# Performance work log

Hardware: AMD Instinct MI355X
Metric: run time of the kernel (lower is better)

The kernel has to match this reference:

```python
import jax, jax.numpy as jnp
import numpy as np

N_NODES = 50000
N_EDGES = 1600000
ATOM_F = 64
FP_SIZE = 2048
N_GRAPHS = 2000


def setup_inputs() -> dict:
    key = jax.random.key(0)
    ks = jax.random.split(key, 12)
    s = 1.0 / np.sqrt(ATOM_F)
    x = jax.random.normal(ks[0], (N_NODES, ATOM_F), dtype=jnp.float32)
    H1_w = jax.random.normal(ks[1], (ATOM_F, ATOM_F), dtype=jnp.float32) * s
    H1_b = jnp.zeros((ATOM_F,), dtype=jnp.float32)
    W1_w = jax.random.normal(ks[2], (FP_SIZE, ATOM_F), dtype=jnp.float32) * s
    W1_b = jnp.zeros((FP_SIZE,), dtype=jnp.float32)
    H2_w = jax.random.normal(ks[3], (ATOM_F, ATOM_F), dtype=jnp.float32) * s
    H2_b = jnp.zeros((ATOM_F,), dtype=jnp.float32)
    W2_w = jax.random.normal(ks[4], (FP_SIZE, ATOM_F), dtype=jnp.float32) * s
    W2_b = jnp.zeros((FP_SIZE,), dtype=jnp.float32)
    edge_index = jax.random.randint(ks[5], (2, N_EDGES), 0, N_NODES, dtype=jnp.int64)
    batch = jnp.sort(jax.random.randint(ks[6], (N_NODES,), 0, N_GRAPHS, dtype=jnp.int64))
    return {
        "x": x,
        "H1_w": H1_w, "H1_b": H1_b, "W1_w": W1_w, "W1_b": W1_b,
        "H2_w": H2_w, "H2_b": H2_b, "W2_w": W2_w, "W2_b": W2_b,
        "edge_index": edge_index,
        "batch": batch,
        "num_graphs": N_GRAPHS,
    }


def reference(x, H1_w, H1_b, W1_w, W1_b, H2_w, H2_b, W2_w, W2_b,
              edge_index, batch, num_graphs):
    n = x.shape[0]
    src, dst = edge_index[0], edge_index[1]

    def loop(h, Hw, Hb, Ww, Wb):
        # sum aggregation over incoming edges; '+ h' accounts for add_self_loops
        agg = jax.ops.segment_sum(h[src], dst, num_segments=n) + h
        upd = jax.nn.sigmoid(agg @ Hw.T + Hb)          # [N, atom_features]
        fp = jax.nn.softmax(upd @ Ww.T + Wb, axis=-1)  # [N, fp_size]
        return upd, fp

    h1, fp1 = loop(x, H1_w, H1_b, W1_w, W1_b)
    _, fp2 = loop(h1, H2_w, H2_b, W2_w, W2_b)
    fingerprint = fp1 + fp2
    # pool per-node fingerprints into per-graph fingerprints
    return jax.ops.segment_sum(fingerprint, batch, num_segments=num_graphs)
```

## Files before the change

### kernel.cpp

```cpp
#include <hip/hip_runtime.h>
#include <hip/hip_bf16.h>

#define AF 64
#define NFP 2048
#define MAXG 4

typedef __attribute__((ext_vector_type(8))) short bf16x8;
typedef __attribute__((ext_vector_type(4))) float f32x4;

__device__ __forceinline__ ushort f2bf(float f) {
    unsigned u = __float_as_uint(f);
    return (ushort)((u + 0x7FFF + ((u >> 16) & 1)) >> 16);
}
__device__ __forceinline__ float bf2f(ushort u) {
    return __uint_as_float((unsigned)u << 16);
}

__global__ __launch_bounds__(256) void hist_kernel(
    const int* __restrict__ keys, int* __restrict__ counts, int n)
{
    int e = blockIdx.x * 256 + threadIdx.x;
    if (e < n) atomicAdd(&counts[keys[e]], 1);
}

__global__ __launch_bounds__(256) void hist_part_kernel(
    const int* __restrict__ dst, int* __restrict__ counts,
    int n_edges, int npr, int nchunks)
{
    int r = blockIdx.x & 7;
    int c = blockIdx.x >> 3;
    int lo = r * npr, hi = lo + npr;
    int per = (n_edges + nchunks - 1) / nchunks;
    int e0 = c * per;
    int e1 = e0 + per; if (e1 > n_edges) e1 = n_edges;
    for (int e = e0 + (int)threadIdx.x; e < e1; e += 256) {
        int d = dst[e];
        if (d >= lo && d < hi) atomicAdd(&counts[d], 1);
    }
}

__global__ __launch_bounds__(1024) void scan_kernel(int* data, int n)
{
    __shared__ int wsum[16];
    __shared__ int chunk_total;
    int t = threadIdx.x, lane = t & 63, w = t >> 6;
    int running = 0;
    for (int base = 0; base < n; base += 1024) {
        int i = base + t;
        int v = (i < n) ? data[i] : 0;
        int x = v;
        #pragma unroll
        for (int off = 1; off < 64; off <<= 1) {
            int y = __shfl_up(x, off);
            if (lane >= off) x += y;
        }
        if (lane == 63) wsum[w] = x;
        __syncthreads();
        if (t == 0) {
            int s = 0;
            #pragma unroll
            for (int q = 0; q < 16; ++q) { int tmp = wsum[q]; wsum[q] = s; s += tmp; }
            chunk_total = s;
        }
        __syncthreads();
        if (i < n) data[i] = x - v + wsum[w] + running;
        running += chunk_total;
        __syncthreads();
    }
    if (t == 0) data[n] = running;
}

__global__ __launch_bounds__(256) void scatter_part_kernel(
    const int* __restrict__ src, const int* __restrict__ dst,
    int* __restrict__ cursor, int* __restrict__ esrc,
    int n_edges, int npr, int nchunks)
{
    int r = blockIdx.x & 7;
    int c = blockIdx.x >> 3;
    int lo = r * npr, hi = lo + npr;
    int per = (n_edges + nchunks - 1) / nchunks;
    int e0 = c * per;
    int e1 = e0 + per; if (e1 > n_edges) e1 = n_edges;
    for (int e = e0 + (int)threadIdx.x; e < e1; e += 256) {
        int d = dst[e];
        if (d >= lo && d < hi) {
            int pos = atomicAdd(&cursor[d], 1);
            esrc[pos] = src[e];
        }
    }
}

__global__ __launch_bounds__(256) void f2bf_kernel(
    const float* __restrict__ W, ushort* __restrict__ Wbf, int n)
{
    int i = blockIdx.x * 256 + threadIdx.x;
    if (i < n) Wbf[i] = f2bf(W[i]);
}

__global__ __launch_bounds__(256) void agg_mlp_kernel(
    const ushort* __restrict__ hbf, const int* __restrict__ offsets,
    const int* __restrict__ esrc, const float* __restrict__ Hw,
    const float* __restrict__ Hb, ushort* __restrict__ outbf, int n_nodes)
{
    __shared__ float Hw_s[AF * 65];
    __shared__ __align__(16) float part[4][8][AF];
    __shared__ float a_red[4][AF];
    __shared__ float hb_s[AF];

    int t = threadIdx.x;
    for (int idx = t; idx < AF * AF; idx += 256) {
        int j = idx >> 6, k = idx & 63;
        Hw_s[j * 65 + k] = Hw[idx];
    }
    if (t < AF) hb_s[t] = Hb[t];

    int w = t >> 6, lane = t & 63;
    int sub = lane >> 3, f8 = lane & 7;
    int i = blockIdx.x * 4 + w;

    float acc[8] = {0.f, 0.f, 0.f, 0.f, 0.f, 0.f, 0.f, 0.f};
    if (i < n_nodes) {
        int o0 = offsets[i], o1 = offsets[i + 1];
        const int* ep = esrc + o0;
        int deg = o1 - o0;
        for (int j = 0; j < deg; j += 8) {
            int jj = j + sub;
            if (jj < deg) {
                int s = ep[jj];
                bf16x8 v = *(const bf16x8*)(hbf + (size_t)s * AF + f8 * 8);
                #pragma unroll
                for (int q = 0; q < 8; ++q) acc[q] += bf2f((ushort)v[q]);
            }
        }
    }
    *(float4*)&part[w][sub][f8 * 8]     = make_float4(acc[0], acc[1], acc[2], acc[3]);
    *(float4*)&part[w][sub][f8 * 8 + 4] = make_float4(acc[4], acc[5], acc[6], acc[7]);
    __syncthreads();

    if (i < n_nodes) {
        float val = bf2f(hbf[(size_t)i * AF + lane]);
        #pragma unroll
        for (int s8 = 0; s8 < 8; ++s8) val += part[w][s8][lane];
        a_red[w][lane] = val;
    }
    __syncthreads();

    if (i < n_nodes) {
        float z = hb_s[lane];
        #pragma unroll
        for (int k = 0; k < AF; ++k)
            z = fmaf(a_red[w][k], Hw_s[lane * 65 + k], z);
        float sg = 1.f / (1.f + __expf(-z));
        outbf[(size_t)i * AF + lane] = f2bf(sg);
    }
}

__global__ __launch_bounds__(256) void fp_node_pool_kernel(
    const ushort* __restrict__ updbf, const ushort* __restrict__ Wbf,
    const float* __restrict__ Wb, const int* __restrict__ batch,
    float* __restrict__ partial, float* __restrict__ out, int n_nodes)
{
    __shared__ float red[4][32];
    __shared__ float sden_s[32];
    __shared__ int   bat_s[32];
    __shared__ __align__(16) float pacc[MAXG][NFP];

    int t = threadIdx.x, wave = t >> 6, lane = t & 63;
    int G = lane >> 4, sl = lane & 15;
    int cw = wave * 512;
    int b = blockIdx.x;
    int i0 = b * 32;

    bf16x8 a00, a01, a10, a11;
    {
        const ushort* p0 = updbf + (size_t)(i0 + sl) * AF + G * 8;
        a00 = *(const bf16x8*)p0;
        a01 = *(const bf16x8*)(p0 + 32);
        const ushort* p1 = updbf + (size_t)(i0 + 16 + sl) * AF + G * 8;
        a10 = *(const bf16x8*)p1;
        a11 = *(const bf16x8*)(p1 + 32);
    }

    float s0[4] = {0.f, 0.f, 0.f, 0.f};
    float s1[4] = {0.f, 0.f, 0.f, 0.f};
    {
        const ushort* wp0 = Wbf + (size_t)(cw + sl) * AF + G * 8;
        bf16x8 nb0 = *(const bf16x8*)wp0;
        bf16x8 nb1 = *(const bf16x8*)(wp0 + 32);
        #pragma unroll 4
        for (int ct = 0; ct < 32; ++ct) {
            bf16x8 b0 = nb0, b1 = nb1;
            if (ct < 31) {
                const ushort* wp = Wbf + (size_t)(cw + (ct + 1) * 16 + sl) * AF + G * 8;
                nb0 = *(const bf16x8*)wp;
                nb1 = *(const bf16x8*)(wp + 32);
            }
            float bias = Wb[cw + ct * 16 + sl];
            f32x4 d0 = {0.f, 0.f, 0.f, 0.f};
            d0 = __builtin_amdgcn_mfma_f32_16x16x32_bf16(a00, b0, d0, 0, 0, 0);
            d0 = __builtin_amdgcn_mfma_f32_16x16x32_bf16(a01, b1, d0, 0, 0, 0);
            f32x4 d1 = {0.f, 0.f, 0.f, 0.f};
            d1 = __builtin_amdgcn_mfma_f32_16x16x32_bf16(a10, b0, d1, 0, 0, 0);
            d1 = __builtin_amdgcn_mfma_f32_16x16x32_bf16(a11, b1, d1, 0, 0, 0);
            #pragma unroll
            for (int r = 0; r < 4; ++r) {
                s0[r] += __expf(d0[r] + bias);
                s1[r] += __expf(d1[r] + bias);
            }
        }
    }
    #pragma unroll
    for (int mask = 1; mask <= 8; mask <<= 1) {
        #pragma unroll
        for (int r = 0; r < 4; ++r) {
            s0[r] += __shfl_xor(s0[r], mask);
            s1[r] += __shfl_xor(s1[r], mask);
        }
    }
    if (sl == 0) {
        #pragma unroll
        for (int r = 0; r < 4; ++r) {
            red[wave][G * 4 + r]      = s0[r];
            red[wave][16 + G * 4 + r] = s1[r];
        }
    }
    if (t < 32) {
        int n = i0 + t;
        bat_s[t] = batch[n < n_nodes ? n : (n_nodes - 1)];
    }
    __syncthreads();
    if (t < 32) {
        float s = red[0][t] + red[1][t] + red[2][t] + red[3][t];
        sden_s[t] = 1.f / s;
    }
    __syncthreads();

    int g_first = bat_s[0];
    int ng = bat_s[31] - g_first + 1;
    int ngl = ng < MAXG ? ng : MAXG;

    for (int gi = 0; gi < ngl; ++gi) {
        *(float4*)&pacc[gi][cw + lane * 8]     = make_float4(0.f, 0.f, 0.f, 0.f);
        *(float4*)&pacc[gi][cw + lane * 8 + 4] = make_float4(0.f, 0.f, 0.f, 0.f);
    }

    float sc0[4], sc1[4];
    int gl0[4], gl1[4];
    #pragma unroll
    for (int r = 0; r < 4; ++r) {
        int l0 = G * 4 + r, l1 = l0 + 16;
        sc0[r] = (i0 + l0 < n_nodes) ? sden_s[l0] : 0.f;
        sc1[r] = (i0 + l1 < n_nodes) ? sden_s[l1] : 0.f;
        gl0[r] = bat_s[l0];
        gl1[r] = bat_s[l1];
    }

    {
        const ushort* wp0 = Wbf + (size_t)(cw + sl) * AF + G * 8;
        bf16x8 nb0 = *(const bf16x8*)wp0;
        bf16x8 nb1 = *(const bf16x8*)(wp0 + 32);
        #pragma unroll 4
        for (int ct = 0; ct < 32; ++ct) {
            bf16x8 b0 = nb0, b1 = nb1;
            if (ct < 31) {
                const ushort* wp = Wbf + (size_t)(cw + (ct + 1) * 16 + sl) * AF + G * 8;
                nb0 = *(const bf16x8*)wp;
                nb1 = *(const bf16x8*)(wp + 32);
            }
            int col = cw + ct * 16 + sl;
            float bias = Wb[col];
            f32x4 d0 = {0.f, 0.f, 0.f, 0.f};
            d0 = __builtin_amdgcn_mfma_f32_16x16x32_bf16(a00, b0, d0, 0, 0, 0);
            d0 = __builtin_amdgcn_mfma_f32_16x16x32_bf16(a01, b1, d0, 0, 0, 0);
            f32x4 d1 = {0.f, 0.f, 0.f, 0.f};
            d1 = __builtin_amdgcn_mfma_f32_16x16x32_bf16(a10, b0, d1, 0, 0, 0);
            d1 = __builtin_amdgcn_mfma_f32_16x16x32_bf16(a11, b1, d1, 0, 0, 0);
            float e0[4], e1[4];
            #pragma unroll
            for (int r = 0; r < 4; ++r) {
                e0[r] = __expf(d0[r] + bias) * sc0[r];
                e1[r] = __expf(d1[r] + bias) * sc1[r];
            }
            for (int gi = 0; gi < ng; ++gi) {
                int g = g_first + gi;
                float c = 0.f;
                #pragma unroll
                for (int r = 0; r < 4; ++r) {
                    c += (gl0[r] == g) ? e0[r] : 0.f;
                    c += (gl1[r] == g) ? e1[r] : 0.f;
                }
                c += __shfl_xor(c, 16);
                c += __shfl_xor(c, 32);
                if (gi < MAXG) {
                    if (G == 0) pacc[gi][col] += c;
                } else if (G == 0) {
                    unsafeAtomicAdd(&out[(size_t)g * NFP + col], c);
                }
            }
        }
    }

    for (int gi = 0; gi < ng; ++gi) {
        float* row = partial + (size_t)(b + g_first + gi) * NFP;
        if (gi < MAXG) {
            *(float4*)&row[cw + lane * 8]     = *(float4*)&pacc[gi][cw + lane * 8];
            *(float4*)&row[cw + lane * 8 + 4] = *(float4*)&pacc[gi][cw + lane * 8 + 4];
        } else {
            *(float4*)&row[cw + lane * 8]     = make_float4(0.f, 0.f, 0.f, 0.f);
            *(float4*)&row[cw + lane * 8 + 4] = make_float4(0.f, 0.f, 0.f, 0.f);
        }
    }
}

__global__ __launch_bounds__(256) void fp_reduce_kernel(
    const float* __restrict__ partial, const int* __restrict__ goff,
    float* __restrict__ out)
{
    int g = blockIdx.x, t = threadIdx.x;
    int gs = goff[g], ge = goff[g + 1];
    if (ge <= gs) return;
    int b0 = gs >> 5, b1 = (ge - 1) >> 5;
    float4 acc0 = make_float4(0.f, 0.f, 0.f, 0.f);
    float4 acc1 = make_float4(0.f, 0.f, 0.f, 0.f);
    for (int b = b0; b <= b1; ++b) {
        const float* row = partial + (size_t)(b + g) * NFP;
        float4 v0 = *(const float4*)&row[t * 8];
        float4 v1 = *(const float4*)&row[t * 8 + 4];
        acc0.x += v0.x; acc0.y += v0.y; acc0.z += v0.z; acc0.w += v0.w;
        acc1.x += v1.x; acc1.y += v1.y; acc1.z += v1.z; acc1.w += v1.w;
    }
    float* po = &out[(size_t)g * NFP];
    float4 o0 = *(float4*)&po[t * 8];
    float4 o1 = *(float4*)&po[t * 8 + 4];
    o0.x += acc0.x; o0.y += acc0.y; o0.z += acc0.z; o0.w += acc0.w;
    o1.x += acc1.x; o1.y += acc1.y; o1.z += acc1.z; o1.w += acc1.w;
    *(float4*)&po[t * 8]     = o0;
    *(float4*)&po[t * 8 + 4] = o1;
}

extern "C" void kernel_launch(void* const* d_in, const int* in_sizes, int n_in,
                              void* d_out, int out_size, void* d_ws, size_t ws_size,
                              hipStream_t stream)
{
    const float* x    = (const float*)d_in[0];
    const float* H1_w = (const float*)d_in[1];
    const float* H1_b = (const float*)d_in[2];
    const float* W1_w = (const float*)d_in[3];
    const float* W1_b = (const float*)d_in[4];
    const float* H2_w = (const float*)d_in[5];
    const float* H2_b = (const float*)d_in[6];
    const float* W2_w = (const float*)d_in[7];
    const float* W2_b = (const float*)d_in[8];
    const int*   ei   = (const int*)d_in[9];
    const int*   batch= (const int*)d_in[10];

    const int n_nodes  = in_sizes[0] / AF;
    const int n_edges  = in_sizes[9] / 2;
    const int n_graphs = out_size / NFP;
    const int npad     = ((n_nodes + 127) / 128) * 128;
    const int* src = ei;
    const int* dst = ei + n_edges;
    float* out = (float*)d_out;

    const int fp_blocks = (n_nodes + 31) / 32;
    const int npairs    = fp_blocks + n_graphs + 1;

    ushort* xbf     = (ushort*)d_ws;
    ushort* ubf1    = xbf  + (size_t)npad * AF;
    ushort* ubf2    = ubf1 + (size_t)npad * AF;
    ushort* Wbf1    = ubf2 + (size_t)npad * AF;
    ushort* Wbf2    = Wbf1 + (size_t)NFP * AF;
    float*  partial = (float*)(Wbf2 + (size_t)NFP * AF);
    int*    offsets = (int*)(partial + (size_t)npairs * NFP);
    int*    cursor  = offsets + (n_nodes + 1);
    int*    goff    = cursor + (n_nodes + 1);
    int*    esrc    = goff + (n_graphs + 1);

    const int nb = (n_nodes + 255) / 256;
    const int mlp_blocks = (n_nodes + 3) / 4;
    const int wn = NFP * AF;
    const int xn = n_nodes * AF;
    const int npr = (n_nodes + 7) / 8;
    const int nchunks = 256;

    f2bf_kernel<<<(xn + 255) / 256, 256, 0, stream>>>(x, xbf, xn);
    f2bf_kernel<<<(wn + 255) / 256, 256, 0, stream>>>(W1_w, Wbf1, wn);
    f2bf_kernel<<<(wn + 255) / 256, 256, 0, stream>>>(W2_w, Wbf2, wn);
    hipMemsetAsync(out, 0, (size_t)out_size * sizeof(float), stream);
    hipMemsetAsync(xbf + (size_t)n_nodes * AF, 0,
                   (size_t)(npad - n_nodes) * AF * sizeof(ushort), stream);
    hipMemsetAsync(ubf1 + (size_t)n_nodes * AF, 0,
                   (size_t)(npad - n_nodes) * AF * sizeof(ushort), stream);
    hipMemsetAsync(ubf2 + (size_t)n_nodes * AF, 0,
                   (size_t)(npad - n_nodes) * AF * sizeof(ushort), stream);
    hipMemsetAsync(offsets, 0, (size_t)(n_nodes + 1) * sizeof(int), stream);
    hipMemsetAsync(goff, 0, (size_t)(n_graphs + 1) * sizeof(int), stream);
    hist_part_kernel<<<nchunks * 8, 256, 0, stream>>>(dst, offsets, n_edges, npr, nchunks);
    hist_kernel<<<nb, 256, 0, stream>>>(batch, goff, n_nodes);
    scan_kernel<<<1, 1024, 0, stream>>>(offsets, n_nodes);
    scan_kernel<<<1, 1024, 0, stream>>>(goff, n_graphs);
    hipMemcpyAsync(cursor, offsets, (size_t)n_nodes * sizeof(int),
                   hipMemcpyDeviceToDevice, stream);
    scatter_part_kernel<<<nchunks * 8, 256, 0, stream>>>(src, dst, cursor, esrc,
                                                         n_edges, npr, nchunks);

    agg_mlp_kernel<<<mlp_blocks, 256, 0, stream>>>(xbf, offsets, esrc,
                                                   H1_w, H1_b, ubf1, n_nodes);
    fp_node_pool_kernel<<<fp_blocks, 256, 0, stream>>>(ubf1, Wbf1, W1_b, batch,
                                                       partial, out, n_nodes);
    fp_reduce_kernel<<<n_graphs, 256, 0, stream>>>(partial, goff, out);

    agg_mlp_kernel<<<mlp_blocks, 256, 0, stream>>>(ubf1, offsets, esrc,
                                                   H2_w, H2_b, ubf2, n_nodes);
    fp_node_pool_kernel<<<fp_blocks, 256, 0, stream>>>(ubf2, Wbf2, W2_b, batch,
                                                       partial, out, n_nodes);
    fp_reduce_kernel<<<n_graphs, 256, 0, stream>>>(partial, goff, out);
}
```

Before: 647.7 us.

## Cache softmax exponentials in registers and pool via segmented LDS atomics

The fingerprint kernel now keeps the per-column exponentials in registers (16x4 per lane) instead of running the MFMA and exp a second time in a second pass. Blocks shrink to 16 nodes with 512 threads (8 waves of 256 columns each). LOG2E is folded into the bf16 weights and the bias so exp2 can be used directly. Per-graph pooling becomes a run-length merge of consecutive same-graph rows followed by LDS atomics, replacing the shuffle-reduce loop. Risks are higher register pressure from the 64-float cache and more partial rows from doubling the block count.

```diff
diff --git a/kernel.cpp b/kernel.cpp
--- a/kernel.cpp
+++ b/kernel.cpp
@@ -4,6 +4,7 @@
 #define AF 64
 #define NFP 2048
 #define MAXG 4
+#define LOG2E 1.4426950408889634f
 
 typedef __attribute__((ext_vector_type(8))) short bf16x8;
 typedef __attribute__((ext_vector_type(4))) float f32x4;
@@ -91,10 +92,10 @@
 }
 
 __global__ __launch_bounds__(256) void f2bf_kernel(
-    const float* __restrict__ W, ushort* __restrict__ Wbf, int n)
+    const float* __restrict__ W, ushort* __restrict__ Wbf, float scale, int n)
 {
     int i = blockIdx.x * 256 + threadIdx.x;
-    if (i < n) Wbf[i] = f2bf(W[i]);
+    if (i < n) Wbf[i] = f2bf(W[i] * scale);
 }
 
 __global__ __launch_bounds__(256) void agg_mlp_kernel(
@@ -155,160 +156,129 @@
     }
 }
 
-__global__ __launch_bounds__(256) void fp_node_pool_kernel(
+__global__ __launch_bounds__(512, 2) void fp_node_pool_kernel(
     const ushort* __restrict__ updbf, const ushort* __restrict__ Wbf,
     const float* __restrict__ Wb, const int* __restrict__ batch,
     float* __restrict__ partial, float* __restrict__ out, int n_nodes)
 {
-    __shared__ float red[4][32];
-    __shared__ float sden_s[32];
-    __shared__ int   bat_s[32];
-    __shared__ __align__(16) float pacc[MAXG][NFP];
+    __shared__ float red[8][16];
+    __shared__ float sden_s[16];
+    __shared__ int   bat_s[16];
+    __shared__ __align__(16) float pacc[MAXG][NFP + 8];
 
     int t = threadIdx.x, wave = t >> 6, lane = t & 63;
     int G = lane >> 4, sl = lane & 15;
-    int cw = wave * 512;
+    int cw = wave * 256;
     int b = blockIdx.x;
-    int i0 = b * 32;
-
-    bf16x8 a00, a01, a10, a11;
+    int i0 = b * 16;
+
+    bf16x8 a0, a1;
     {
         const ushort* p0 = updbf + (size_t)(i0 + sl) * AF + G * 8;
-        a00 = *(const bf16x8*)p0;
-        a01 = *(const bf16x8*)(p0 + 32);
-        const ushort* p1 = updbf + (size_t)(i0 + 16 + sl) * AF + G * 8;
-        a10 = *(const bf16x8*)p1;
-        a11 = *(const bf16x8*)(p1 + 32);
+        a0 = *(const bf16x8*)p0;
+        a1 = *(const bf16x8*)(p0 + 32);
+    }
+    if (t < 16) {
+        int n = i0 + t;
+        bat_s[t] = batch[n < n_nodes ? n : (n_nodes - 1)];
     }
 
     float s0[4] = {0.f, 0.f, 0.f, 0.f};
-    float s1[4] = {0.f, 0.f, 0.f, 0.f};
+    float ef[16][4];
     {
         const ushort* wp0 = Wbf + (size_t)(cw + sl) * AF + G * 8;
         bf16x8 nb0 = *(const bf16x8*)wp0;
         bf16x8 nb1 = *(const bf16x8*)(wp0 + 32);
-        #pragma unroll 4
-        for (int ct = 0; ct < 32; ++ct) {
+        #pragma unroll
+        for (int ct = 0; ct < 16; ++ct) {
             bf16x8 b0 = nb0, b1 = nb1;
-            if (ct < 31) {
+            if (ct < 15) {
                 const ushort* wp = Wbf + (size_t)(cw + (ct + 1) * 16 + sl) * AF + G * 8;
                 nb0 = *(const bf16x8*)wp;
                 nb1 = *(const bf16x8*)(wp + 32);
             }
-            float bias = Wb[cw + ct * 16 + sl];
+            float bias = Wb[cw + ct * 16 + sl] * LOG2E;
             f32x4 d0 = {0.f, 0.f, 0.f, 0.f};
-            d0 = __builtin_amdgcn_mfma_f32_16x16x32_bf16(a00, b0, d0, 0, 0, 0);
-            d0 = __builtin_amdgcn_mfma_f32_16x16x32_bf16(a01, b1, d0, 0, 0, 0);
-            f32x4 d1 = {0.f, 0.f, 0.f, 0.f};
-            d1 = __builtin_amdgcn_mfma_f32_16x16x32_bf16(a10, b0, d1, 0, 0, 0);
-            d1 = __builtin_amdgcn_mfma_f32_16x16x32_bf16(a11, b1, d1, 0, 0, 0);
+            d0 = __builtin_amdgcn_mfma_f32_16x16x32_bf16(a0, b0, d0, 0, 0, 0);
+            d0 = __builtin_amdgcn_mfma_f32_16x16x32_bf16(a1, b1, d0, 0, 0, 0);
             #pragma unroll
             for (int r = 0; r < 4; ++r) {
-                s0[r] += __expf(d0[r] + bias);
-                s1[r] += __expf(d1[r] + bias);
+                float e = __builtin_amdgcn_exp2f(d0[r] + bias);
+                ef[ct][r] = e;
+                s0[r] += e;
             }
         }
     }
     #pragma unroll
     for (int mask = 1; mask <= 8; mask <<= 1) {
         #pragma unroll
-        for (int r = 0; r < 4; ++r) {
-            s0[r] += __shfl_xor(s0[r], mask);
-            s1[r] += __shfl_xor(s1[r], mask);
-        }
+        for (int r = 0; r < 4; ++r) s0[r] += __shfl_xor(s0[r], mask);
     }
     if (sl == 0) {
         #pragma unroll
-        for (int r = 0; r < 4; ++r) {
-            red[wave][G * 4 + r]      = s0[r];
-            red[wave][16 + G * 4 + r] = s1[r];
-        }
-    }
-    if (t < 32) {
-        int n = i0 + t;
-        bat_s[t] = batch[n < n_nodes ? n : (n_nodes - 1)];
+        for (int r = 0; r < 4; ++r) red[wave][G * 4 + r] = s0[r];
     }
     __syncthreads();
-    if (t < 32) {
-        float s = red[0][t] + red[1][t] + red[2][t] + red[3][t];
+    if (t < 16) {
+        float s = 0.f;
+        #pragma unroll
+        for (int w8 = 0; w8 < 8; ++w8) s += red[w8][t];
         sden_s[t] = 1.f / s;
     }
     __syncthreads();
 
     int g_first = bat_s[0];
-    int ng = bat_s[31] - g_first + 1;
+    int ng = bat_s[15] - g_first + 1;
     int ngl = ng < MAXG ? ng : MAXG;
 
-    for (int gi = 0; gi < ngl; ++gi) {
-        *(float4*)&pacc[gi][cw + lane * 8]     = make_float4(0.f, 0.f, 0.f, 0.f);
-        *(float4*)&pacc[gi][cw + lane * 8 + 4] = make_float4(0.f, 0.f, 0.f, 0.f);
-    }
-
-    float sc0[4], sc1[4];
-    int gl0[4], gl1[4];
+    for (int gi = 0; gi < ngl; ++gi)
+        *(float4*)&pacc[gi][cw + lane * 4] = make_float4(0.f, 0.f, 0.f, 0.f);
+
+    float sc0[4];
+    int rel0[4];
     #pragma unroll
     for (int r = 0; r < 4; ++r) {
-        int l0 = G * 4 + r, l1 = l0 + 16;
+        int l0 = G * 4 + r;
         sc0[r] = (i0 + l0 < n_nodes) ? sden_s[l0] : 0.f;
-        sc1[r] = (i0 + l1 < n_nodes) ? sden_s[l1] : 0.f;
-        gl0[r] = bat_s[l0];
-        gl1[r] = bat_s[l1];
-    }
-
-    {
-        const ushort* wp0 = Wbf + (size_t)(cw + sl) * AF + G * 8;
-        bf16x8 nb0 = *(const bf16x8*)wp0;
-        bf16x8 nb1 = *(const bf16x8*)(wp0 + 32);
-        #pragma unroll 4
-        for (int ct = 0; ct < 32; ++ct) {
-            bf16x8 b0 = nb0, b1 = nb1;
-            if (ct < 31) {
-                const ushort* wp = Wbf + (size_t)(cw + (ct + 1) * 16 + sl) * AF + G * 8;
-                nb0 = *(const bf16x8*)wp;
-                nb1 = *(const bf16x8*)(wp + 32);
-            }
-            int col = cw + ct * 16 + sl;
-            float bias = Wb[col];
-            f32x4 d0 = {0.f, 0.f, 0.f, 0.f};
-            d0 = __builtin_amdgcn_mfma_f32_16x16x32_bf16(a00, b0, d0, 0, 0, 0);
-            d0 = __builtin_amdgcn_mfma_f32_16x16x32_bf16(a01, b1, d0, 0, 0, 0);
-            f32x4 d1 = {0.f, 0.f, 0.f, 0.f};
-            d1 = __builtin_amdgcn_mfma_f32_16x16x32_bf16(a10, b0, d1, 0, 0, 0);
-            d1 = __builtin_amdgcn_mfma_f32_16x16x32_bf16(a11, b1, d1, 0, 0, 0);
-            float e0[4], e1[4];
-            #pragma unroll
-            for (int r = 0; r < 4; ++r) {
-                e0[r] = __expf(d0[r] + bias) * sc0[r];
-                e1[r] = __expf(d1[r] + bias) * sc1[r];
-            }
-            for (int gi = 0; gi < ng; ++gi) {
-                int g = g_first + gi;
-                float c = 0.f;
-                #pragma unroll
-                for (int r = 0; r < 4; ++r) {
-                    c += (gl0[r] == g) ? e0[r] : 0.f;
-                    c += (gl1[r] == g) ? e1[r] : 0.f;
-                }
-                c += __shfl_xor(c, 16);
-                c += __shfl_xor(c, 32);
-                if (gi < MAXG) {
-                    if (G == 0) pacc[gi][col] += c;
-                } else if (G == 0) {
-                    unsafeAtomicAdd(&out[(size_t)g * NFP + col], c);
-                }
-            }
-        }
+        rel0[r] = bat_s[l0] - g_first;
+    }
+    bool m0a = (rel0[1] == rel0[0]);
+    bool m0b = (rel0[2] == rel0[1]);
+    bool m0c = (rel0[3] == rel0[2]);
+
+    #pragma unroll
+    for (int ct = 0; ct < 16; ++ct) {
+        int col = cw + ct * 16 + sl;
+        float f0 = ef[ct][0] * sc0[0];
+        float f1 = ef[ct][1] * sc0[1];
+        float f2 = ef[ct][2] * sc0[2];
+        float f3 = ef[ct][3] * sc0[3];
+
+        float run = f0;
+        if (!m0a) {
+            if (rel0[0] < MAXG) atomicAdd(&pacc[rel0[0]][col], run);
+            else unsafeAtomicAdd(&out[(size_t)(g_first + rel0[0]) * NFP + col], run);
+            run = f1;
+        } else run += f1;
+        if (!m0b) {
+            if (rel0[1] < MAXG) atomicAdd(&pacc[rel0[1]][col], run);
+            else unsafeAtomicAdd(&out[(size_t)(g_first + rel0[1]) * NFP + col], run);
+            run = f2;
+        } else run += f2;
+        if (!m0c) {
+            if (rel0[2] < MAXG) atomicAdd(&pacc[rel0[2]][col], run);
+            else unsafeAtomicAdd(&out[(size_t)(g_first + rel0[2]) * NFP + col], run);
+            run = f3;
+        } else run += f3;
+        if (rel0[3] < MAXG) atomicAdd(&pacc[rel0[3]][col], run);
+        else unsafeAtomicAdd(&out[(size_t)(g_first + rel0[3]) * NFP + col], run);
     }
 
     for (int gi = 0; gi < ng; ++gi) {
         float* row = partial + (size_t)(b + g_first + gi) * NFP;
-        if (gi < MAXG) {
-            *(float4*)&row[cw + lane * 8]     = *(float4*)&pacc[gi][cw + lane * 8];
-            *(float4*)&row[cw + lane * 8 + 4] = *(float4*)&pacc[gi][cw + lane * 8 + 4];
-        } else {
-            *(float4*)&row[cw + lane * 8]     = make_float4(0.f, 0.f, 0.f, 0.f);
-            *(float4*)&row[cw + lane * 8 + 4] = make_float4(0.f, 0.f, 0.f, 0.f);
-        }
+        float4 v = make_float4(0.f, 0.f, 0.f, 0.f);
+        if (gi < MAXG) v = *(float4*)&pacc[gi][cw + lane * 4];
+        *(float4*)&row[cw + lane * 4] = v;
     }
 }
 
@@ -319,7 +289,7 @@
     int g = blockIdx.x, t = threadIdx.x;
     int gs = goff[g], ge = goff[g + 1];
     if (ge <= gs) return;
-    int b0 = gs >> 5, b1 = (ge - 1) >> 5;
+    int b0 = gs >> 4, b1 = (ge - 1) >> 4;
     float4 acc0 = make_float4(0.f, 0.f, 0.f, 0.f);
     float4 acc1 = make_float4(0.f, 0.f, 0.f, 0.f);
     for (int b = b0; b <= b1; ++b) {
@@ -362,7 +332,7 @@
     const int* dst = ei + n_edges;
     float* out = (float*)d_out;
 
-    const int fp_blocks = (n_nodes + 31) / 32;
+    const int fp_blocks = (n_nodes + 15) / 16;
     const int npairs    = fp_blocks + n_graphs + 1;
 
     ushort* xbf     = (ushort*)d_ws;
@@ -383,9 +353,9 @@
     const int npr = (n_nodes + 7) / 8;
     const int nchunks = 256;
 
-    f2bf_kernel<<<(xn + 255) / 256, 256, 0, stream>>>(x, xbf, xn);
-    f2bf_kernel<<<(wn + 255) / 256, 256, 0, stream>>>(W1_w, Wbf1, wn);
-    f2bf_kernel<<<(wn + 255) / 256, 256, 0, stream>>>(W2_w, Wbf2, wn);
+    f2bf_kernel<<<(xn + 255) / 256, 256, 0, stream>>>(x, xbf, 1.0f, xn);
+    f2bf_kernel<<<(wn + 255) / 256, 256, 0, stream>>>(W1_w, Wbf1, LOG2E, wn);
+    f2bf_kernel<<<(wn + 255) / 256, 256, 0, stream>>>(W2_w, Wbf2, LOG2E, wn);
     hipMemsetAsync(out, 0, (size_t)out_size * sizeof(float), stream);
     hipMemsetAsync(xbf + (size_t)n_nodes * AF, 0,
                    (size_t)(npad - n_nodes) * AF * sizeof(ushort), stream);
@@ -406,13 +376,13 @@
 
     agg_mlp_kernel<<<mlp_blocks, 256, 0, stream>>>(xbf, offsets, esrc,
                                                    H1_w, H1_b, ubf1, n_nodes);
-    fp_node_pool_kernel<<<fp_blocks, 256, 0, stream>>>(ubf1, Wbf1, W1_b, batch,
+    fp_node_pool_kernel<<<fp_blocks, 512, 0, stream>>>(ubf1, Wbf1, W1_b, batch,
                                                        partial, out, n_nodes);
     fp_reduce_kernel<<<n_graphs, 256, 0, stream>>>(partial, goff, out);
 
     agg_mlp_kernel<<<mlp_blocks, 256, 0, stream>>>(ubf1, offsets, esrc,
                                                    H2_w, H2_b, ubf2, n_nodes);
-    fp_node_pool_kernel<<<fp_blocks, 256, 0, stream>>>(ubf2, Wbf2, W2_b, batch,
+    fp_node_pool_kernel<<<fp_blocks, 512, 0, stream>>>(ubf2, Wbf2, W2_b, batch,
                                                        partial, out, n_nodes);
     fp_reduce_kernel<<<n_graphs, 256, 0, stream>>>(partial, goff, out);
 }
```

Result: slower. 781.5 us (+20.6%).

## Parallelize offset scan across blocks and fold log2e into weights for exp2

Applied to the files above, without the earlier changes.

The single-block scan over all node degree counts is replaced by a three-kernel multi-block scan: per-block scan, scan of block sums, then an add pass. This removes a serial 50k-element loop running on one workgroup. Separately, the fingerprint weights and biases are prescaled by log2(e) so the softmax exponent uses the native exp2 instruction instead of __expf. The bf16 rounding of the prescaled weights shifts numerics slightly, and the scan adds two extra launches.

```diff
diff --git a/kernel.cpp b/kernel.cpp
--- a/kernel.cpp
+++ b/kernel.cpp
@@ -4,6 +4,7 @@
 #define AF 64
 #define NFP 2048
 #define MAXG 4
+#define LOG2E 1.4426950408889634f
 
 typedef __attribute__((ext_vector_type(8))) short bf16x8;
 typedef __attribute__((ext_vector_type(4))) float f32x4;
@@ -68,6 +69,62 @@
         __syncthreads();
     }
     if (t == 0) data[n] = running;
+}
+
+__global__ __launch_bounds__(1024) void scan_block_kernel(
+    int* __restrict__ data, int* __restrict__ bsum, int n)
+{
+    __shared__ int wsum[16];
+    int t = threadIdx.x, lane = t & 63, w = t >> 6;
+    int i = blockIdx.x * 1024 + t;
+    int v = (i < n) ? data[i] : 0;
+    int x = v;
+    #pragma unroll
+    for (int off = 1; off < 64; off <<= 1) {
+        int y = __shfl_up(x, off);
+        if (lane >= off) x += y;
+    }
+    if (lane == 63) wsum[w] = x;
+    __syncthreads();
+    if (t == 0) {
+        int s = 0;
+        #pragma unroll
+        for (int q = 0; q < 16; ++q) { int tmp = wsum[q]; wsum[q] = s; s += tmp; }
+        bsum[blockIdx.x] = s;
+    }
+    __syncthreads();
+    if (i < n) data[i] = x - v + wsum[w];
+}
+
+__global__ __launch_bounds__(1024) void scan_sums_kernel(int* bsum, int nb)
+{
+    __shared__ int wsum[16];
+    int t = threadIdx.x, lane = t & 63, w = t >> 6;
+    int v = (t < nb) ? bsum[t] : 0;
+    int x = v;
+    #pragma unroll
+    for (int off = 1; off < 64; off <<= 1) {
+        int y = __shfl_up(x, off);
+        if (lane >= off) x += y;
+    }
+    if (lane == 63) wsum[w] = x;
+    __syncthreads();
+    if (t == 0) {
+        int s = 0;
+        #pragma unroll
+        for (int q = 0; q < 16; ++q) { int tmp = wsum[q]; wsum[q] = s; s += tmp; }
+        bsum[nb] = s;
+    }
+    __syncthreads();
+    if (t < nb) bsum[t] = x - v + wsum[w];
+}
+
+__global__ __launch_bounds__(256) void scan_add_kernel(
+    int* __restrict__ data, const int* __restrict__ bsum, int n, int nb)
+{
+    int i = blockIdx.x * 256 + threadIdx.x;
+    if (i < n) data[i] += bsum[i >> 10];
+    if (i == 0) data[n] = bsum[nb];
 }
 
 __global__ __launch_bounds__(256) void scatter_part_kernel(
@@ -91,10 +148,10 @@
 }
 
 __global__ __launch_bounds__(256) void f2bf_kernel(
-    const float* __restrict__ W, ushort* __restrict__ Wbf, int n)
+    const float* __restrict__ W, ushort* __restrict__ Wbf, float scale, int n)
 {
     int i = blockIdx.x * 256 + threadIdx.x;
-    if (i < n) Wbf[i] = f2bf(W[i]);
+    if (i < n) Wbf[i] = f2bf(W[i] * scale);
 }
 
 __global__ __launch_bounds__(256) void agg_mlp_kernel(
@@ -195,7 +252,7 @@
                 nb0 = *(const bf16x8*)wp;
                 nb1 = *(const bf16x8*)(wp + 32);
             }
-            float bias = Wb[cw + ct * 16 + sl];
+            float bias = Wb[cw + ct * 16 + sl] * LOG2E;
             f32x4 d0 = {0.f, 0.f, 0.f, 0.f};
             d0 = __builtin_amdgcn_mfma_f32_16x16x32_bf16(a00, b0, d0, 0, 0, 0);
             d0 = __builtin_amdgcn_mfma_f32_16x16x32_bf16(a01, b1, d0, 0, 0, 0);
@@ -204,8 +261,8 @@
             d1 = __builtin_amdgcn_mfma_f32_16x16x32_bf16(a11, b1, d1, 0, 0, 0);
             #pragma unroll
             for (int r = 0; r < 4; ++r) {
-                s0[r] += __expf(d0[r] + bias);
-                s1[r] += __expf(d1[r] + bias);
+                s0[r] += __builtin_amdgcn_exp2f(d0[r] + bias);
+                s1[r] += __builtin_amdgcn_exp2f(d1[r] + bias);
             }
         }
     }
@@ -268,7 +325,7 @@
                 nb1 = *(const bf16x8*)(wp + 32);
             }
             int col = cw + ct * 16 + sl;
-            float bias = Wb[col];
+            float bias = Wb[col] * LOG2E;
             f32x4 d0 = {0.f, 0.f, 0.f, 0.f};
             d0 = __builtin_amdgcn_mfma_f32_16x16x32_bf16(a00, b0, d0, 0, 0, 0);
             d0 = __builtin_amdgcn_mfma_f32_16x16x32_bf16(a01, b1, d0, 0, 0, 0);
@@ -278,8 +335,8 @@
             float e0[4], e1[4];
             #pragma unroll
             for (int r = 0; r < 4; ++r) {
-                e0[r] = __expf(d0[r] + bias) * sc0[r];
-                e1[r] = __expf(d1[r] + bias) * sc1[r];
+                e0[r] = __builtin_amdgcn_exp2f(d0[r] + bias) * sc0[r];
+                e1[r] = __builtin_amdgcn_exp2f(d1[r] + bias) * sc1[r];
             }
             for (int gi = 0; gi < ng; ++gi) {
                 int g = g_first + gi;
@@ -364,6 +421,7 @@
 
     const int fp_blocks = (n_nodes + 31) / 32;
     const int npairs    = fp_blocks + n_graphs + 1;
+    const int nsb       = (n_nodes + 1023) / 1024;
 
     ushort* xbf     = (ushort*)d_ws;
     ushort* ubf1    = xbf  + (size_t)npad * AF;
@@ -374,7 +432,8 @@
     int*    offsets = (int*)(partial + (size_t)npairs * NFP);
     int*    cursor  = offsets + (n_nodes + 1);
     int*    goff    = cursor + (n_nodes + 1);
-    int*    esrc    = goff + (n_graphs + 1);
+    int*    bscan   = goff + (n_graphs + 1);
+    int*    esrc    = bscan + (nsb + 1);
 
     const int nb = (n_nodes + 255) / 256;
     const int mlp_blocks = (n_nodes + 3) / 4;
@@ -383,9 +442,9 @@
     const int npr = (n_nodes + 7) / 8;
     const int nchunks = 256;
 
-    f2bf_kernel<<<(xn + 255) / 256, 256, 0, stream>>>(x, xbf, xn);
-    f2bf_kernel<<<(wn + 255) / 256, 256, 0, stream>>>(W1_w, Wbf1, wn);
-    f2bf_kernel<<<(wn + 255) / 256, 256, 0, stream>>>(W2_w, Wbf2, wn);
+    f2bf_kernel<<<(xn + 255) / 256, 256, 0, stream>>>(x, xbf, 1.0f, xn);
+    f2bf_kernel<<<(wn + 255) / 256, 256, 0, stream>>>(W1_w, Wbf1, LOG2E, wn);
+    f2bf_kernel<<<(wn + 255) / 256, 256, 0, stream>>>(W2_w, Wbf2, LOG2E, wn);
     hipMemsetAsync(out, 0, (size_t)out_size * sizeof(float), stream);
     hipMemsetAsync(xbf + (size_t)n_nodes * AF, 0,
                    (size_t)(npad - n_nodes) * AF * sizeof(ushort), stream);
@@ -397,7 +456,10 @@
     hipMemsetAsync(goff, 0, (size_t)(n_graphs + 1) * sizeof(int), stream);
     hist_part_kernel<<<nchunks * 8, 256, 0, stream>>>(dst, offsets, n_edges, npr, nchunks);
     hist_kernel<<<nb, 256, 0, stream>>>(batch, goff, n_nodes);
-    scan_kernel<<<1, 1024, 0, stream>>>(offsets, n_nodes);
+    scan_block_kernel<<<nsb, 1024, 0, stream>>>(offsets, bscan, n_nodes);
+    scan_sums_kernel<<<1, 1024, 0, stream>>>(bscan, nsb);
+    scan_add_kernel<<<(n_nodes + 255) / 256, 256, 0, stream>>>(offsets, bscan,
+                                                               n_nodes, nsb);
     scan_kernel<<<1, 1024, 0, stream>>>(goff, n_graphs);
     hipMemcpyAsync(cursor, offsets, (size_t)n_nodes * sizeof(int),
                    hipMemcpyDeviceToDevice, stream);
```

New measurement: 612.5 us. -5.4%, faster.
